# Optimization experiments

Measured on AMD Instinct MI355X. Metric: run time of the kernel, lower is better.

Reference implementation:

```python
import jax, jax.numpy as jnp
import numpy as np

N_NODES = 800_000
N_FRAGS = 100_000
N_ROOTS = 2_000
NODE_FEATS = 86
HIDDEN = 128
MAX_BROKEN = 6
OUT_DIM = MAX_BROKEN * 2 + 1  # 13
MLP_IN = HIDDEN * 3 + OUT_DIM  # 397


def _lin_init(key, fan_in, fan_out):
    k1, k2 = jax.random.split(key)
    bound = 1.0 / np.sqrt(fan_in)
    W = jax.random.uniform(k1, (fan_in, fan_out), jnp.float32, -bound, bound)
    b = jax.random.uniform(k2, (fan_out,), jnp.float32, -bound, bound)
    return W, b


def setup_inputs() -> dict:
    key = jax.random.key(0)
    ks = jax.random.split(key, 16)
    node_h = jax.random.normal(ks[0], (N_NODES, NODE_FEATS), jnp.float32)
    segment_ids = jnp.sort(jax.random.randint(ks[1], (N_NODES,), 0, N_FRAGS))
    root_repr = jax.random.normal(ks[2], (N_ROOTS, NODE_FEATS), jnp.float32)
    ind_maps = jax.random.randint(ks[3], (N_FRAGS,), 0, N_ROOTS)
    broken = jax.random.randint(ks[4], (N_FRAGS,), 0, OUT_DIM)
    W_root, b_root = _lin_init(ks[5], NODE_FEATS, HIDDEN)
    W_in, b_in = _lin_init(ks[6], NODE_FEATS, HIDDEN)
    W_g1, b_g1 = _lin_init(ks[7], HIDDEN, HIDDEN)
    W_g2, b_g2 = _lin_init(ks[8], HIDDEN, HIDDEN)
    W_m1, b_m1 = _lin_init(ks[9], MLP_IN, HIDDEN)
    W_m2, b_m2 = _lin_init(ks[10], HIDDEN, HIDDEN)
    W_out, b_out = _lin_init(ks[11], HIDDEN, OUT_DIM)
    W_attn, b_attn = _lin_init(ks[12], HIDDEN, OUT_DIM)
    return dict(node_h=node_h, segment_ids=segment_ids, root_repr=root_repr,
                ind_maps=ind_maps, broken=broken,
                W_root=W_root, b_root=b_root, W_in=W_in, b_in=b_in,
                W_g1=W_g1, b_g1=b_g1, W_g2=W_g2, b_g2=b_g2,
                W_m1=W_m1, b_m1=b_m1, W_m2=W_m2, b_m2=b_m2,
                W_out=W_out, b_out=b_out, W_attn=W_attn, b_attn=b_attn)


def _segment_mean(x, seg_ids, num_segments):
    sums = jax.ops.segment_sum(x, seg_ids, num_segments=num_segments)
    counts = jax.ops.segment_sum(jnp.ones((x.shape[0],), x.dtype), seg_ids,
                                 num_segments=num_segments)
    return sums / jnp.maximum(counts, 1.0)[:, None]


def reference(node_h, segment_ids, root_repr, ind_maps, broken,
              W_root, b_root, W_in, b_in, W_g1, b_g1, W_g2, b_g2,
              W_m1, b_m1, W_m2, b_m2, W_out, b_out, W_attn, b_attn):
    # root encoder: Linear + ReLU (dropout=0)
    root_emb = jax.nn.relu(root_repr @ W_root + b_root)        # [R, H]
    ext_root = root_emb[ind_maps]                              # [F, H] gather
    # node input + 2 GNN (nodewise Linear+ReLU fallback) layers
    frag_h = node_h @ W_in + b_in                              # [N, H]
    frag_h = jax.nn.relu(frag_h @ W_g1 + b_g1)
    frag_h = jax.nn.relu(frag_h @ W_g2 + b_g2)
    # ragged mean-pool per fragment graph (dgl.mean_nodes)
    avg_frags = _segment_mean(frag_h, segment_ids, N_FRAGS)    # [F, H]
    # one-hot of clamped broken-bond counts
    broken_oh = jax.nn.one_hot(jnp.clip(broken, 0, MAX_BROKEN * 2), OUT_DIM,
                               dtype=frag_h.dtype)             # [F, 13]
    cat = jnp.concatenate([ext_root, ext_root - avg_frags, avg_frags,
                           broken_oh], axis=-1)                # [F, 397]
    hidden = jax.nn.relu(jax.nn.relu(cat @ W_m1 + b_m1) @ W_m2 + b_m2)
    output = jax.nn.sigmoid(hidden @ W_out + b_out)            # [F, 13]
    attn_weights = hidden @ W_attn + b_attn                    # [F, 13]
    return output, attn_weights
```

## Files before the change

### kernel.cpp

```cpp
#include <hip/hip_runtime.h>
#include <math.h>

typedef __attribute__((ext_vector_type(8))) short short8;
typedef __attribute__((ext_vector_type(4))) float float4v;

#define AST 136
#define CST 424

__device__ __forceinline__ unsigned short f2bf(float f) {
    union { float f; unsigned u; } v; v.f = f;
    return (unsigned short)((v.u + 0x7fffu + ((v.u >> 16) & 1u)) >> 16);
}
__device__ __forceinline__ float bf2f(unsigned v) {
    union { unsigned u; float f; } x; x.u = v << 16; return x.f;
}

template<int KP>
__device__ __forceinline__ void layer2t(const unsigned short* X, int astr,
                                        const unsigned short* __restrict__ WT,
                                        const float* __restrict__ bias,
                                        int lane, int tb, float4v acc[4][2])
{
    const int col0 = lane & 15, q = lane >> 4;
#pragma unroll
    for (int t = 0; t < 2; ++t) {
        float b = bias[(tb + t) * 16 + col0];
#pragma unroll
        for (int mt = 0; mt < 4; ++mt) acc[mt][t] = (float4v){b, b, b, b};
    }
#pragma unroll
    for (int ks = 0; ks < KP; ks += 32) {
        const int k0 = ks + q * 8;
        short8 B[2];
#pragma unroll
        for (int t = 0; t < 2; ++t)
            B[t] = *(const short8*)(WT + (size_t)((tb + t) * 16 + col0) * KP + k0);
#pragma unroll
        for (int mt = 0; mt < 4; ++mt) {
            short8 A = *(const short8*)(X + (mt * 16 + col0) * astr + k0);
#pragma unroll
            for (int t = 0; t < 2; ++t)
                acc[mt][t] = __builtin_amdgcn_mfma_f32_16x16x32_bf16(A, B[t], acc[mt][t], 0, 0, 0);
        }
    }
}

__device__ __forceinline__ void store2t(float4v acc[4][2], unsigned short* Y,
                                        int lane, int tb, bool relu)
{
    const int col0 = lane & 15, q = lane >> 4;
#pragma unroll
    for (int mt = 0; mt < 4; ++mt)
#pragma unroll
        for (int t = 0; t < 2; ++t)
#pragma unroll
            for (int r = 0; r < 4; ++r) {
                float v = acc[mt][t][r];
                if (relu) v = fmaxf(v, 0.0f);
                Y[(mt * 16 + q * 4 + r) * AST + (tb + t) * 16 + col0] = f2bf(v);
            }
}

__global__ void prep_kernel(const float* __restrict__ W_in, const float* __restrict__ W_g1,
                            const float* __restrict__ W_g2, const float* __restrict__ W_m1,
                            const float* __restrict__ W_m2, const float* __restrict__ W_out,
                            const float* __restrict__ W_attn, unsigned short* __restrict__ wt)
{
    int i = blockIdx.x * 256 + threadIdx.x;
    unsigned short* WT_in = wt;
    unsigned short* WT_g1 = WT_in + 12288;
    unsigned short* WT_g2 = WT_g1 + 16384;
    unsigned short* WT_m1 = WT_g2 + 16384;
    unsigned short* WT_m2 = WT_m1 + 53248;
    unsigned short* WT_h  = WT_m2 + 16384;
    if (i < 12288) { int n = i / 96, k = i - n * 96;
        WT_in[i] = (k < 86) ? f2bf(W_in[k * 128 + n]) : 0; return; }
    i -= 12288;
    if (i < 16384) { int n = i >> 7, k = i & 127;
        WT_g1[i] = f2bf(W_g1[k * 128 + n]); return; }
    i -= 16384;
    if (i < 16384) { int n = i >> 7, k = i & 127;
        WT_g2[i] = f2bf(W_g2[k * 128 + n]); return; }
    i -= 16384;
    if (i < 53248) { int n = i / 416, k = i - n * 416;
        WT_m1[i] = (k < 397) ? f2bf(W_m1[k * 128 + n]) : 0; return; }
    i -= 53248;
    if (i < 16384) { int n = i >> 7, k = i & 127;
        WT_m2[i] = f2bf(W_m2[k * 128 + n]); return; }
    i -= 16384;
    if (i < 4096) { int n = i >> 7, k = i & 127;
        WT_h[i] = (n < 13) ? f2bf(W_out[k * 13 + n])
                           : (n < 26 ? f2bf(W_attn[k * 13 + (n - 13)]) : 0); }
}

__global__ void root_kernel(const float* __restrict__ root_repr,
                            const float* __restrict__ W_root,
                            const float* __restrict__ b_root,
                            float* __restrict__ root_emb)
{
    __shared__ float x[86];
    const int r = blockIdx.x, tid = threadIdx.x;
    if (tid < 86) x[tid] = root_repr[(size_t)r * 86 + tid];
    __syncthreads();
    float acc = b_root[tid];
    for (int k = 0; k < 86; ++k)
        acc = fmaf(x[k], W_root[k * 128 + tid], acc);
    root_emb[(size_t)r * 128 + tid] = fmaxf(acc, 0.0f);
}

__global__ __launch_bounds__(256, 4)
void node_kernel(const float* __restrict__ node_h, const int* __restrict__ seg_ids,
                 const unsigned short* __restrict__ WT_in, const float* __restrict__ b_in,
                 const unsigned short* __restrict__ WT_g1, const float* __restrict__ b_g1,
                 const unsigned short* __restrict__ WT_g2, const float* __restrict__ b_g2,
                 float* __restrict__ frag_sum, float* __restrict__ frag_cnt)
{
    __shared__ __align__(16) unsigned short X[64 * AST];
    __shared__ __align__(16) unsigned short Y[64 * AST];
    __shared__ int segs[64];
    const int tid = threadIdx.x, wv = tid >> 6, lane = tid & 63, tb = wv * 2;
    const long n0 = (long)blockIdx.x * 64;

    if (tid < 64) segs[tid] = seg_ids[n0 + tid];
    {
        const float4* src = (const float4*)(node_h + n0 * 86);
#pragma unroll
        for (int j = 0; j < 6; ++j) {
            int i4 = j * 256 + tid;
            if (i4 < 1376) {
                float4 v = src[i4];
                int e = i4 << 2;
                int n = e / 86, k = e - n * 86;
                X[n * AST + k] = f2bf(v.x);
                int e1 = e + 1; n = e1 / 86; k = e1 - n * 86; X[n * AST + k] = f2bf(v.y);
                int e2 = e + 2; n = e2 / 86; k = e2 - n * 86; X[n * AST + k] = f2bf(v.z);
                int e3 = e + 3; n = e3 / 86; k = e3 - n * 86; X[n * AST + k] = f2bf(v.w);
            }
        }
        for (int idx = tid; idx < 640; idx += 256) {
            int n = idx / 10, k = idx - n * 10;
            X[n * AST + 86 + k] = 0;
        }
    }
    __syncthreads();

    float4v acc[4][2];
    layer2t<96>(X, AST, WT_in, b_in, lane, tb, acc);
    store2t(acc, Y, lane, tb, false);
    __syncthreads();
    layer2t<128>(Y, AST, WT_g1, b_g1, lane, tb, acc);
    store2t(acc, X, lane, tb, true);
    __syncthreads();
    layer2t<128>(X, AST, WT_g2, b_g2, lane, tb, acc);
    store2t(acc, Y, lane, tb, true);
    __syncthreads();

    {
        const int col = tid & 127, half = tid >> 7, r0 = half << 5;
        const int prevSeg = (half == 1) ? segs[31] : -1;
        const int nextSeg = (half == 0) ? segs[32] : -1;
        int cur = segs[r0], runStart = r0;
        float sum = 0.f, cnt = 0.f;
        for (int n = r0; n < r0 + 32; ++n) {
            int s = segs[n];
            if (s != cur) {
                bool bnd = (runStart == r0) && (half == 0 || prevSeg == cur);
                if (bnd) atomicAdd(&frag_sum[(size_t)cur * 128 + col], sum);
                else     frag_sum[(size_t)cur * 128 + col] = sum;
                if (col == 0) {
                    if (bnd) atomicAdd(&frag_cnt[cur], cnt);
                    else     frag_cnt[cur] = cnt;
                }
                sum = 0.f; cnt = 0.f; cur = s; runStart = n;
            }
            sum += bf2f((unsigned)Y[n * AST + col]);
            cnt += 1.f;
        }
        bool bnd = ((runStart == r0) && (half == 0 || prevSeg == cur))
                   || (half == 1) || (nextSeg == cur);
        if (bnd) atomicAdd(&frag_sum[(size_t)cur * 128 + col], sum);
        else     frag_sum[(size_t)cur * 128 + col] = sum;
        if (col == 0) {
            if (bnd) atomicAdd(&frag_cnt[cur], cnt);
            else     frag_cnt[cur] = cnt;
        }
    }
}

__global__ __launch_bounds__(256, 2)
void frag_kernel(const float* __restrict__ root_emb, const float* __restrict__ frag_sum,
                 const float* __restrict__ frag_cnt, const int* __restrict__ ind_maps,
                 const int* __restrict__ broken,
                 const unsigned short* __restrict__ WT_m1, const float* __restrict__ b_m1,
                 const unsigned short* __restrict__ WT_m2, const float* __restrict__ b_m2,
                 const unsigned short* __restrict__ WT_h,
                 const float* __restrict__ b_out, const float* __restrict__ b_attn,
                 float* __restrict__ out0, float* __restrict__ out1)
{
    __shared__ __align__(16) unsigned short cat[64 * CST];
    __shared__ __align__(16) unsigned short Y[64 * AST];
    unsigned short* X2 = cat;
    const int tid = threadIdx.x, wv = tid >> 6, lane = tid & 63, tb = wv * 2;
    const int col0 = lane & 15, q = lane >> 4;
    const long f0 = (long)blockIdx.x * 64;

    {
        const int m = tid >> 2, j = tid & 3;
        int fc = (int)f0 + m; if (fc > 99999) fc = 99999;
        const int rid = ind_maps[fc];
        const float inv = 1.0f / fmaxf(frag_cnt[fc], 1.0f);
        unsigned short* row = cat + m * CST;
#pragma unroll
        for (int jj = 0; jj < 8; ++jj) {
            int k = j * 32 + jj * 4;
            float4 e = *(const float4*)(root_emb + (size_t)rid * 128 + k);
            float4 s = *(const float4*)(frag_sum + (size_t)fc * 128 + k);
            float sx = s.x * inv, sy = s.y * inv, sz = s.z * inv, sw = s.w * inv;
            row[k]     = f2bf(e.x); row[k + 1] = f2bf(e.y);
            row[k + 2] = f2bf(e.z); row[k + 3] = f2bf(e.w);
            row[128 + k]     = f2bf(e.x - sx); row[128 + k + 1] = f2bf(e.y - sy);
            row[128 + k + 2] = f2bf(e.z - sz); row[128 + k + 3] = f2bf(e.w - sw);
            row[256 + k]     = f2bf(sx); row[256 + k + 1] = f2bf(sy);
            row[256 + k + 2] = f2bf(sz); row[256 + k + 3] = f2bf(sw);
        }
        if (j == 3) {
            int b = broken[fc]; b = b < 0 ? 0 : (b > 12 ? 12 : b);
            for (int kk = 0; kk < 32; ++kk)
                row[384 + kk] = (kk == b) ? 0x3f80 : 0;
        }
    }
    __syncthreads();

    float4v acc[4][2];
    layer2t<416>(cat, CST, WT_m1, b_m1, lane, tb, acc);
    store2t(acc, Y, lane, tb, true);
    __syncthreads();
    layer2t<128>(Y, AST, WT_m2, b_m2, lane, tb, acc);
    store2t(acc, X2, lane, tb, true);
    __syncthreads();

    float4v hacc[2];
#pragma unroll
    for (int t = 0; t < 2; ++t) {
        int cc = t * 16 + col0;
        float b = cc < 13 ? b_out[cc] : (cc < 26 ? b_attn[cc - 13] : 0.0f);
        hacc[t] = (float4v){b, b, b, b};
    }
#pragma unroll
    for (int ks = 0; ks < 128; ks += 32) {
        const int k0 = ks + q * 8;
        short8 A = *(const short8*)(X2 + (wv * 16 + col0) * AST + k0);
#pragma unroll
        for (int t = 0; t < 2; ++t) {
            short8 B = *(const short8*)(WT_h + (t * 16 + col0) * 128 + k0);
            hacc[t] = __builtin_amdgcn_mfma_f32_16x16x32_bf16(A, B, hacc[t], 0, 0, 0);
        }
    }
#pragma unroll
    for (int t = 0; t < 2; ++t)
#pragma unroll
        for (int r = 0; r < 4; ++r) {
            long ff = f0 + wv * 16 + q * 4 + r;
            int cc = t * 16 + col0;
            if (ff < 100000) {
                float v = hacc[t][r];
                if (cc < 13)      out0[ff * 13 + cc] = 1.0f / (1.0f + expf(-v));
                else if (cc < 26) out1[ff * 13 + cc - 13] = v;
            }
        }
}

extern "C" void kernel_launch(void* const* d_in, const int* in_sizes, int n_in,
                              void* d_out, int out_size, void* d_ws, size_t ws_size,
                              hipStream_t stream)
{
    const float* node_h    = (const float*)d_in[0];
    const int*   seg_ids   = (const int*)d_in[1];
    const float* root_repr = (const float*)d_in[2];
    const int*   ind_maps  = (const int*)d_in[3];
    const int*   broken    = (const int*)d_in[4];
    const float* W_root = (const float*)d_in[5];  const float* b_root = (const float*)d_in[6];
    const float* W_in   = (const float*)d_in[7];  const float* b_in   = (const float*)d_in[8];
    const float* W_g1   = (const float*)d_in[9];  const float* b_g1   = (const float*)d_in[10];
    const float* W_g2   = (const float*)d_in[11]; const float* b_g2   = (const float*)d_in[12];
    const float* W_m1   = (const float*)d_in[13]; const float* b_m1   = (const float*)d_in[14];
    const float* W_m2   = (const float*)d_in[15]; const float* b_m2   = (const float*)d_in[16];
    const float* W_out  = (const float*)d_in[17]; const float* b_out  = (const float*)d_in[18];
    const float* W_attn = (const float*)d_in[19]; const float* b_attn = (const float*)d_in[20];

    char* ws = (char*)d_ws;
    float* root_emb = (float*)ws;
    float* frag_sum = (float*)(ws + 1024000);
    float* frag_cnt = (float*)(ws + 52224000);
    unsigned short* wt = (unsigned short*)(ws + 52624000);
    const unsigned short* WT_in = wt;
    const unsigned short* WT_g1 = wt + 12288;
    const unsigned short* WT_g2 = WT_g1 + 16384;
    const unsigned short* WT_m1 = WT_g2 + 16384;
    const unsigned short* WT_m2 = WT_m1 + 53248;
    const unsigned short* WT_h  = WT_m2 + 16384;

    hipMemsetAsync(frag_sum, 0, 51600000, stream);

    float* out0 = (float*)d_out;
    float* out1 = out0 + (size_t)100000 * 13;

    prep_kernel<<<464, 256, 0, stream>>>(W_in, W_g1, W_g2, W_m1, W_m2, W_out, W_attn, wt);
    root_kernel<<<2000, 128, 0, stream>>>(root_repr, W_root, b_root, root_emb);
    node_kernel<<<12500, 256, 0, stream>>>(node_h, seg_ids, WT_in, b_in,
                                           WT_g1, b_g1, WT_g2, b_g2, frag_sum, frag_cnt);
    frag_kernel<<<1563, 256, 0, stream>>>(root_emb, frag_sum, frag_cnt, ind_maps, broken,
                                          WT_m1, b_m1, WT_m2, b_m2, WT_h, b_out, b_attn,
                                          out0, out1);
}
```

Baseline: 585.1 us.

## Give each wave its own 16 rows and chain layers without block barriers

Reworks the MFMA tiling so each wave owns 16 rows and computes all 128 output columns, using transposed MFMA (weights as A, activations as B). Intermediate activations stay wave-private in one shared buffer, which removes the inter-layer __syncthreads and halves node-kernel LDS. The first layer in both kernels now builds its bf16 operand directly from global memory (node_h, and root_emb/frag_sum/one-hot) instead of staging a concat tile in LDS. In exchange each wave reloads the full weight matrix, and the node_h row loads are strided and uncoalesced; frag_kernel occupancy hint is raised to 3.

After: 946.6 us. 1.62x slower.

```diff
diff --git a/kernel.cpp b/kernel.cpp
--- a/kernel.cpp
+++ b/kernel.cpp
@@ -3,9 +3,9 @@
 
 typedef __attribute__((ext_vector_type(8))) short short8;
 typedef __attribute__((ext_vector_type(4))) float float4v;
+typedef __attribute__((ext_vector_type(4))) unsigned short ushort4v;
 
 #define AST 136
-#define CST 424
 
 __device__ __forceinline__ unsigned short f2bf(float f) {
     union { float f; unsigned u; } v; v.f = f;
@@ -16,49 +16,41 @@
 }
 
 template<int KP>
-__device__ __forceinline__ void layer2t(const unsigned short* X, int astr,
-                                        const unsigned short* __restrict__ WT,
-                                        const float* __restrict__ bias,
-                                        int lane, int tb, float4v acc[4][2])
-{
-    const int col0 = lane & 15, q = lane >> 4;
-#pragma unroll
-    for (int t = 0; t < 2; ++t) {
-        float b = bias[(tb + t) * 16 + col0];
-#pragma unroll
-        for (int mt = 0; mt < 4; ++mt) acc[mt][t] = (float4v){b, b, b, b};
+__device__ __forceinline__ void layerL(const unsigned short* hrow,
+                                       const unsigned short* __restrict__ WT,
+                                       const float* __restrict__ bias,
+                                       int col0, int q, float4v acc[8])
+{
+#pragma unroll
+    for (int t = 0; t < 8; ++t) {
+        float4 bv = *(const float4*)(bias + t * 16 + q * 4);
+        acc[t] = (float4v){bv.x, bv.y, bv.z, bv.w};
     }
 #pragma unroll
     for (int ks = 0; ks < KP; ks += 32) {
-        const int k0 = ks + q * 8;
-        short8 B[2];
-#pragma unroll
-        for (int t = 0; t < 2; ++t)
-            B[t] = *(const short8*)(WT + (size_t)((tb + t) * 16 + col0) * KP + k0);
-#pragma unroll
-        for (int mt = 0; mt < 4; ++mt) {
-            short8 A = *(const short8*)(X + (mt * 16 + col0) * astr + k0);
-#pragma unroll
-            for (int t = 0; t < 2; ++t)
-                acc[mt][t] = __builtin_amdgcn_mfma_f32_16x16x32_bf16(A, B[t], acc[mt][t], 0, 0, 0);
-        }
-    }
-}
-
-__device__ __forceinline__ void store2t(float4v acc[4][2], unsigned short* Y,
-                                        int lane, int tb, bool relu)
-{
-    const int col0 = lane & 15, q = lane >> 4;
-#pragma unroll
-    for (int mt = 0; mt < 4; ++mt)
-#pragma unroll
-        for (int t = 0; t < 2; ++t)
-#pragma unroll
-            for (int r = 0; r < 4; ++r) {
-                float v = acc[mt][t][r];
-                if (relu) v = fmaxf(v, 0.0f);
-                Y[(mt * 16 + q * 4 + r) * AST + (tb + t) * 16 + col0] = f2bf(v);
-            }
+        short8 Y = *(const short8*)(hrow + ks + q * 8);
+#pragma unroll
+        for (int t = 0; t < 8; ++t) {
+            short8 B = *(const short8*)(WT + (size_t)(t * 16 + col0) * KP + ks + q * 8);
+            acc[t] = __builtin_amdgcn_mfma_f32_16x16x32_bf16(B, Y, acc[t], 0, 0, 0);
+        }
+    }
+}
+
+__device__ __forceinline__ void storeT(float4v acc[8], unsigned short* hrow,
+                                       int q, bool relu)
+{
+#pragma unroll
+    for (int t = 0; t < 8; ++t) {
+        ushort4v p;
+#pragma unroll
+        for (int r = 0; r < 4; ++r) {
+            float v = acc[t][r];
+            if (relu) v = fmaxf(v, 0.0f);
+            p[r] = f2bf(v);
+        }
+        *(ushort4v*)(hrow + t * 16 + q * 4) = p;
+    }
 }
 
 __global__ void prep_kernel(const float* __restrict__ W_in, const float* __restrict__ W_g1,
@@ -115,44 +107,46 @@
                  const unsigned short* __restrict__ WT_g2, const float* __restrict__ b_g2,
                  float* __restrict__ frag_sum, float* __restrict__ frag_cnt)
 {
-    __shared__ __align__(16) unsigned short X[64 * AST];
-    __shared__ __align__(16) unsigned short Y[64 * AST];
+    __shared__ __align__(16) unsigned short h[64 * AST];
     __shared__ int segs[64];
-    const int tid = threadIdx.x, wv = tid >> 6, lane = tid & 63, tb = wv * 2;
+    const int tid = threadIdx.x, wv = tid >> 6, lane = tid & 63;
+    const int col0 = lane & 15, q = lane >> 4;
+    const int row = wv * 16 + col0;
     const long n0 = (long)blockIdx.x * 64;
+    unsigned short* hrow = h + row * AST;
 
     if (tid < 64) segs[tid] = seg_ids[n0 + tid];
+
+    const float* xrow = node_h + (n0 + row) * 86;
+    float4v acc[8];
     {
-        const float4* src = (const float4*)(node_h + n0 * 86);
-#pragma unroll
-        for (int j = 0; j < 6; ++j) {
-            int i4 = j * 256 + tid;
-            if (i4 < 1376) {
-                float4 v = src[i4];
-                int e = i4 << 2;
-                int n = e / 86, k = e - n * 86;
-                X[n * AST + k] = f2bf(v.x);
-                int e1 = e + 1; n = e1 / 86; k = e1 - n * 86; X[n * AST + k] = f2bf(v.y);
-                int e2 = e + 2; n = e2 / 86; k = e2 - n * 86; X[n * AST + k] = f2bf(v.z);
-                int e3 = e + 3; n = e3 / 86; k = e3 - n * 86; X[n * AST + k] = f2bf(v.w);
-            }
-        }
-        for (int idx = tid; idx < 640; idx += 256) {
-            int n = idx / 10, k = idx - n * 10;
-            X[n * AST + 86 + k] = 0;
-        }
-    }
-    __syncthreads();
-
-    float4v acc[4][2];
-    layer2t<96>(X, AST, WT_in, b_in, lane, tb, acc);
-    store2t(acc, Y, lane, tb, false);
-    __syncthreads();
-    layer2t<128>(Y, AST, WT_g1, b_g1, lane, tb, acc);
-    store2t(acc, X, lane, tb, true);
-    __syncthreads();
-    layer2t<128>(X, AST, WT_g2, b_g2, lane, tb, acc);
-    store2t(acc, Y, lane, tb, true);
+#pragma unroll
+        for (int t = 0; t < 8; ++t) {
+            float4 bv = *(const float4*)(b_in + t * 16 + q * 4);
+            acc[t] = (float4v){bv.x, bv.y, bv.z, bv.w};
+        }
+#pragma unroll
+        for (int ks = 0; ks < 96; ks += 32) {
+            const int k0 = ks + q * 8;
+            short8 Y;
+#pragma unroll
+            for (int i = 0; i < 8; ++i) {
+                int k = k0 + i;
+                float v = (k < 86) ? xrow[k] : 0.0f;
+                Y[i] = (short)f2bf(v);
+            }
+#pragma unroll
+            for (int t = 0; t < 8; ++t) {
+                short8 B = *(const short8*)(WT_in + (size_t)(t * 16 + col0) * 96 + k0);
+                acc[t] = __builtin_amdgcn_mfma_f32_16x16x32_bf16(B, Y, acc[t], 0, 0, 0);
+            }
+        }
+    }
+    storeT(acc, hrow, q, false);
+    layerL<128>(hrow, WT_g1, b_g1, col0, q, acc);
+    storeT(acc, hrow, q, true);
+    layerL<128>(hrow, WT_g2, b_g2, col0, q, acc);
+    storeT(acc, hrow, q, true);
     __syncthreads();
 
     {
@@ -173,7 +167,7 @@
                 }
                 sum = 0.f; cnt = 0.f; cur = s; runStart = n;
             }
-            sum += bf2f((unsigned)Y[n * AST + col]);
+            sum += bf2f((unsigned)h[n * AST + col]);
             cnt += 1.f;
         }
         bool bnd = ((runStart == r0) && (half == 0 || prevSeg == cur))
@@ -187,7 +181,7 @@
     }
 }
 
-__global__ __launch_bounds__(256, 2)
+__global__ __launch_bounds__(256, 3)
 void frag_kernel(const float* __restrict__ root_emb, const float* __restrict__ frag_sum,
                  const float* __restrict__ frag_cnt, const int* __restrict__ ind_maps,
                  const int* __restrict__ broken,
@@ -197,77 +191,101 @@
                  const float* __restrict__ b_out, const float* __restrict__ b_attn,
                  float* __restrict__ out0, float* __restrict__ out1)
 {
-    __shared__ __align__(16) unsigned short cat[64 * CST];
-    __shared__ __align__(16) unsigned short Y[64 * AST];
-    unsigned short* X2 = cat;
-    const int tid = threadIdx.x, wv = tid >> 6, lane = tid & 63, tb = wv * 2;
+    __shared__ __align__(16) unsigned short h[64 * AST];
+    const int tid = threadIdx.x, wv = tid >> 6, lane = tid & 63;
     const int col0 = lane & 15, q = lane >> 4;
+    const int row = wv * 16 + col0;
     const long f0 = (long)blockIdx.x * 64;
-
+    unsigned short* hrow = h + row * AST;
+
+    int fc = (int)(f0 + row); if (fc > 99999) fc = 99999;
+    const int rid = ind_maps[fc];
+    const float inv = 1.0f / fmaxf(frag_cnt[fc], 1.0f);
+    int bi = broken[fc]; bi = bi < 0 ? 0 : (bi > 12 ? 12 : bi);
+
+    float4v acc[8];
     {
-        const int m = tid >> 2, j = tid & 3;
-        int fc = (int)f0 + m; if (fc > 99999) fc = 99999;
-        const int rid = ind_maps[fc];
-        const float inv = 1.0f / fmaxf(frag_cnt[fc], 1.0f);
-        unsigned short* row = cat + m * CST;
-#pragma unroll
-        for (int jj = 0; jj < 8; ++jj) {
-            int k = j * 32 + jj * 4;
-            float4 e = *(const float4*)(root_emb + (size_t)rid * 128 + k);
-            float4 s = *(const float4*)(frag_sum + (size_t)fc * 128 + k);
-            float sx = s.x * inv, sy = s.y * inv, sz = s.z * inv, sw = s.w * inv;
-            row[k]     = f2bf(e.x); row[k + 1] = f2bf(e.y);
-            row[k + 2] = f2bf(e.z); row[k + 3] = f2bf(e.w);
-            row[128 + k]     = f2bf(e.x - sx); row[128 + k + 1] = f2bf(e.y - sy);
-            row[128 + k + 2] = f2bf(e.z - sz); row[128 + k + 3] = f2bf(e.w - sw);
-            row[256 + k]     = f2bf(sx); row[256 + k + 1] = f2bf(sy);
-            row[256 + k + 2] = f2bf(sz); row[256 + k + 3] = f2bf(sw);
-        }
-        if (j == 3) {
-            int b = broken[fc]; b = b < 0 ? 0 : (b > 12 ? 12 : b);
-            for (int kk = 0; kk < 32; ++kk)
-                row[384 + kk] = (kk == b) ? 0x3f80 : 0;
-        }
-    }
-    __syncthreads();
-
-    float4v acc[4][2];
-    layer2t<416>(cat, CST, WT_m1, b_m1, lane, tb, acc);
-    store2t(acc, Y, lane, tb, true);
-    __syncthreads();
-    layer2t<128>(Y, AST, WT_m2, b_m2, lane, tb, acc);
-    store2t(acc, X2, lane, tb, true);
-    __syncthreads();
+#pragma unroll
+        for (int t = 0; t < 8; ++t) {
+            float4 bv = *(const float4*)(b_m1 + t * 16 + q * 4);
+            acc[t] = (float4v){bv.x, bv.y, bv.z, bv.w};
+        }
+#pragma unroll
+        for (int ks = 0; ks < 416; ks += 32) {
+            const int k0 = ks + q * 8;
+            float av[8];
+            if (ks >= 384) {
+#pragma unroll
+                for (int i = 0; i < 8; ++i) {
+                    int oh = k0 + i - 384;
+                    av[i] = (oh == bi) ? 1.0f : 0.0f;
+                }
+            } else if (ks < 128) {
+                const float4* e = (const float4*)(root_emb + (size_t)rid * 128 + k0);
+                float4 e0 = e[0], e1 = e[1];
+                av[0] = e0.x; av[1] = e0.y; av[2] = e0.z; av[3] = e0.w;
+                av[4] = e1.x; av[5] = e1.y; av[6] = e1.z; av[7] = e1.w;
+            } else if (ks < 256) {
+                int kk = k0 - 128;
+                const float4* e = (const float4*)(root_emb + (size_t)rid * 128 + kk);
+                const float4* s = (const float4*)(frag_sum + (size_t)fc * 128 + kk);
+                float4 e0 = e[0], e1 = e[1], s0 = s[0], s1 = s[1];
+                av[0] = e0.x - s0.x * inv; av[1] = e0.y - s0.y * inv;
+                av[2] = e0.z - s0.z * inv; av[3] = e0.w - s0.w * inv;
+                av[4] = e1.x - s1.x * inv; av[5] = e1.y - s1.y * inv;
+                av[6] = e1.z - s1.z * inv; av[7] = e1.w - s1.w * inv;
+            } else {
+                int kk = k0 - 256;
+                const float4* s = (const float4*)(frag_sum + (size_t)fc * 128 + kk);
+                float4 s0 = s[0], s1 = s[1];
+                av[0] = s0.x * inv; av[1] = s0.y * inv; av[2] = s0.z * inv; av[3] = s0.w * inv;
+                av[4] = s1.x * inv; av[5] = s1.y * inv; av[6] = s1.z * inv; av[7] = s1.w * inv;
+            }
+            short8 Y;
+#pragma unroll
+            for (int i = 0; i < 8; ++i) Y[i] = (short)f2bf(av[i]);
+#pragma unroll
+            for (int t = 0; t < 8; ++t) {
+                short8 B = *(const short8*)(WT_m1 + (size_t)(t * 16 + col0) * 416 + k0);
+                acc[t] = __builtin_amdgcn_mfma_f32_16x16x32_bf16(B, Y, acc[t], 0, 0, 0);
+            }
+        }
+    }
+    storeT(acc, hrow, q, true);
+    layerL<128>(hrow, WT_m2, b_m2, col0, q, acc);
+    storeT(acc, hrow, q, true);
 
     float4v hacc[2];
 #pragma unroll
     for (int t = 0; t < 2; ++t) {
-        int cc = t * 16 + col0;
-        float b = cc < 13 ? b_out[cc] : (cc < 26 ? b_attn[cc - 13] : 0.0f);
-        hacc[t] = (float4v){b, b, b, b};
+#pragma unroll
+        for (int r = 0; r < 4; ++r) {
+            int cc = t * 16 + q * 4 + r;
+            hacc[t][r] = cc < 13 ? b_out[cc] : (cc < 26 ? b_attn[cc - 13] : 0.0f);
+        }
     }
 #pragma unroll
     for (int ks = 0; ks < 128; ks += 32) {
         const int k0 = ks + q * 8;
-        short8 A = *(const short8*)(X2 + (wv * 16 + col0) * AST + k0);
+        short8 Y = *(const short8*)(hrow + k0);
 #pragma unroll
         for (int t = 0; t < 2; ++t) {
-            short8 B = *(const short8*)(WT_h + (t * 16 + col0) * 128 + k0);
-            hacc[t] = __builtin_amdgcn_mfma_f32_16x16x32_bf16(A, B, hacc[t], 0, 0, 0);
-        }
-    }
-#pragma unroll
-    for (int t = 0; t < 2; ++t)
-#pragma unroll
-        for (int r = 0; r < 4; ++r) {
-            long ff = f0 + wv * 16 + q * 4 + r;
-            int cc = t * 16 + col0;
-            if (ff < 100000) {
+            short8 B = *(const short8*)(WT_h + (size_t)(t * 16 + col0) * 128 + k0);
+            hacc[t] = __builtin_amdgcn_mfma_f32_16x16x32_bf16(B, Y, hacc[t], 0, 0, 0);
+        }
+    }
+    const long ff = f0 + row;
+    if (ff < 100000) {
+#pragma unroll
+        for (int t = 0; t < 2; ++t)
+#pragma unroll
+            for (int r = 0; r < 4; ++r) {
+                int cc = t * 16 + q * 4 + r;
                 float v = hacc[t][r];
                 if (cc < 13)      out0[ff * 13 + cc] = 1.0f / (1.0f + expf(-v));
                 else if (cc < 26) out1[ff * 13 + cc - 13] = v;
             }
-        }
+    }
 }
 
 extern "C" void kernel_launch(void* const* d_in, const int* in_sizes, int n_in,
```
